# Kernel optimization log

Hardware: AMD Instinct MI355X
Metric: run time of the kernel (lower is better)

## Reference

```python
import jax, jax.numpy as jnp
import numpy as np
from jax import lax

H = 16  # hidden size

def lstm_dir(x_tbd, Wih, Whh, bih, bhh):
    # x_tbd: [T, B, D] -> outputs [T, B, H], final h [B, H]
    T, B, _ = x_tbd.shape
    xg = jnp.einsum('tbd,gd->tbg', x_tbd, Wih) + bih + bhh  # [T, B, 4H]
    def step(carry, xt):
        h, c = carry
        g = xt + h @ Whh.T
        i, f, gg, o = jnp.split(g, 4, axis=-1)  # PyTorch gate order i,f,g,o
        i = jax.nn.sigmoid(i); f = jax.nn.sigmoid(f)
        gg = jnp.tanh(gg); o = jax.nn.sigmoid(o)
        c = f * c + i * gg
        h = o * jnp.tanh(c)
        return (h, c), h
    init = (jnp.zeros((B, H), x_tbd.dtype), jnp.zeros((B, H), x_tbd.dtype))
    (hT, cT), hs = lax.scan(step, init, xg)
    return hs, hT

def bi_layer(x_tbd, pf, pb):
    hs_f, hT_f = lstm_dir(x_tbd, *pf)
    hs_b_rev, hT_b = lstm_dir(x_tbd[::-1], *pb)
    out = jnp.concatenate([hs_f, hs_b_rev[::-1]], axis=-1)  # [T, B, 2H]
    return out, hT_f, hT_b


def setup_inputs() -> dict:
    key = jax.random.key(0)
    ks = iter(jax.random.split(key, 32))
    B, T = 4096, 512
    d = {"x": jax.random.normal(next(ks), (B, T), jnp.float32)}
    def w(shape):
        return jax.random.normal(next(ks), shape, jnp.float32) * 0.2
    # layer 0 (input dim 1), forward / backward directions
    for s in ('f', 'b'):
        d[f'Wih0{s}'] = w((4 * H, 1)); d[f'Whh0{s}'] = w((4 * H, H))
        d[f'bih0{s}'] = jnp.zeros((4 * H,), jnp.float32)
        d[f'bhh0{s}'] = jnp.zeros((4 * H,), jnp.float32)
    # layer 1 (input dim 2H = 32)
    for s in ('f', 'b'):
        d[f'Wih1{s}'] = w((4 * H, 2 * H)); d[f'Whh1{s}'] = w((4 * H, H))
        d[f'bih1{s}'] = jnp.zeros((4 * H,), jnp.float32)
        d[f'bhh1{s}'] = jnp.zeros((4 * H,), jnp.float32)
    # MLP head: Linear(32,25), Linear(25,20)
    d['W1'] = w((25, 2 * H)); d['b1'] = jnp.zeros((25,), jnp.float32)
    d['W2'] = w((20, 25)); d['b2'] = jnp.zeros((20,), jnp.float32)
    return d


def reference(x, Wih0f, Whh0f, bih0f, bhh0f, Wih0b, Whh0b, bih0b, bhh0b,
              Wih1f, Whh1f, bih1f, bhh1f, Wih1b, Whh1b, bih1b, bhh1b,
              W1, b1, W2, b2):
    # x: [B, T] -> unsqueeze(2) -> [B, T, 1]; scan over time, so transpose to [T, B, 1]
    x_tbd = x.T[:, :, None]
    o0, _, _ = bi_layer(x_tbd, (Wih0f, Whh0f, bih0f, bhh0f), (Wih0b, Whh0b, bih0b, bhh0b))
    # dropout=0.1 between layers is inactive in eval mode (reference = eval)
    _, hT_f, hT_b = bi_layer(o0, (Wih1f, Whh1f, bih1f, bhh1f), (Wih1b, Whh1b, bih1b, bhh1b))
    # torch: cat((h[-1], h[-2]), 1) = (last-layer backward, last-layer forward)
    feat = jnp.concatenate([hT_b, hT_f], axis=1)  # [B, 32]
    z = jax.nn.elu(feat)
    z = jax.nn.elu(z @ W1.T + b1)
    z = jax.nn.elu(z @ W2.T + b2)
    return z  # [B, 20]
```

## Files before the change

kernel.cpp:

```cpp
#include <hip/hip_runtime.h>
#include <stdint.h>

#define TT 512
#define BB 4096
#define NT8 512
#define LOG2E 1.4426950408889634f

typedef _Float16 half8_t __attribute__((ext_vector_type(8)));
typedef __fp16 fp16x2_t __attribute__((ext_vector_type(2)));
typedef float f32x4 __attribute__((ext_vector_type(4)));
typedef float f32x2 __attribute__((ext_vector_type(2)));

union FragU { uint4 u4; half8_t h8; };
union PkU { fp16x2_t h2; unsigned int u; };

__device__ __forceinline__ float rcp_(float x){ return __builtin_amdgcn_rcpf(x); }
__device__ __forceinline__ float exp2_(float x){ return __builtin_amdgcn_exp2f(x); }
__device__ __forceinline__ float elu_(float x){ return x > 0.0f ? x : (exp2_(x * LOG2E) - 1.0f); }
__device__ __forceinline__ int mini_(int a, int b){ return a < b ? a : b; }
__device__ __forceinline__ float maskhi_(float x){ return __uint_as_float(__float_as_uint(x) & 0xFFFFE000u); }
__device__ __forceinline__ unsigned int pkrtz_(float a, float b){
    PkU p; p.h2 = __builtin_amdgcn_cvt_pkrtz(a, b); return p.u;
}
__device__ __forceinline__ unsigned int pkrne_(float a, float b){
    PkU p; p.h2[0] = (__fp16)a; p.h2[1] = (__fp16)b; return p.u;
}

__device__ __forceinline__ f32x4 MFMA(half8_t a, half8_t b, f32x4 c) {
    return __builtin_amdgcn_mfma_f32_16x16x32_f16(a, b, c, 0, 0, 0);
}

__device__ __forceinline__ f32x4 ld4_(const float* p){ return *(const f32x4*)p; }

__device__ __forceinline__ half8_t packA8s(const float* s, float sc) {
    half8_t h;
#pragma unroll
    for (int k = 0; k < 8; ++k) h[k] = (_Float16)(s[k] * sc);
    return h;
}
__device__ __forceinline__ half8_t zero8_() {
    half8_t h;
#pragma unroll
    for (int k = 0; k < 8; ++k) h[k] = (_Float16)0.0f;
    return h;
}

__device__ __forceinline__ void cell2p_(f32x2 gi, f32x2 gf, f32x2 gg, f32x2 go,
                                        f32x2& c, f32x2& h) {
    f32x2 ei, ef, eg, eo;
    ei[0] = exp2_(-gi[0]); ei[1] = exp2_(-gi[1]);
    ef[0] = exp2_(-gf[0]); ef[1] = exp2_(-gf[1]);
    eg[0] = exp2_(-gg[0]); eg[1] = exp2_(-gg[1]);
    eo[0] = exp2_(-go[0]); eo[1] = exp2_(-go[1]);
    const f32x2 one = {1.0f, 1.0f};
    f32x2 ai = one + ei, af = one + ef, ag = one + eg, ao = one + eo;
    f32x2 pif = ai * af, pgo = ag * ao;
    f32x2 P = pif * pgo;
    f32x2 R; R[0] = rcp_(P[0]); R[1] = rcp_(P[1]);
    f32x2 I = R * (af * pgo);
    f32x2 F = R * (ai * pgo);
    f32x2 Gt = R * (pif * ao);
    f32x2 O = R * (pif * ag);
    f32x2 G = Gt + Gt - one;
    c = F * c + I * G;
    f32x2 ct = c * (-2.0f * LOG2E);
    f32x2 et; et[0] = exp2_(ct[0]); et[1] = exp2_(ct[1]);
    f32x2 den = one + et;
    f32x2 Rt; Rt[0] = rcp_(den[0]); Rt[1] = rcp_(den[1]);
    f32x2 T = Rt + Rt - one;
    h = O * T;
}


struct PA {
    const float *x;
    const float *WihF, *WhhF, *bihF, *bhhF;
    const float *WihB, *WhhB, *bihB, *bhhB;
    char* ws;
};

__global__ __launch_bounds__(256) void phaseA_k(PA p) {
    __shared__ uint4 ldsAll[4 * 16];
    const int tid = threadIdx.x;
    const int lane = tid & 63;
    const int wv   = tid >> 6;
    char* lds = (char*)ldsAll + wv * 256;
    const int q = lane >> 4, b = lane & 15, c = b & 7;
    const bool hi8 = b >= 8;
    const int chain = blockIdx.x * 4 + wv;
    const int tile = chain >> 1, dir = chain & 1;

    const float* Wih = dir ? p.WihB : p.WihF;
    const float* Whh = dir ? p.WhhB : p.WhhF;
    const float* bih = dir ? p.bihB : p.bihF;
    const float* bhh = dir ? p.bhhB : p.bhhF;

    auto mkA = [&](int m, float sc)->half8_t {
        if (q < 2) return packA8s(Whh + (16*m + b)*16 + 8*q, sc);
        half8_t h = zero8_();
        if (q == 2) {
            float w = Wih[16*m + b] * sc;
            h[0] = (_Float16)w;
            h[1] = (_Float16)w;
        }
        return h;
    };
    half8_t A0 = mkA(0, LOG2E);
    half8_t A1 = mkA(1, LOG2E);
    half8_t A2 = mkA(2, 2.0f*LOG2E);
    half8_t A3 = mkA(3, LOG2E);

    f32x4 bias0 = (ld4_(bih +      4*q) + ld4_(bhh +      4*q)) * LOG2E;
    f32x4 bias1 = (ld4_(bih + 16 + 4*q) + ld4_(bhh + 16 + 4*q)) * LOG2E;
    f32x4 bias2 = (ld4_(bih + 32 + 4*q) + ld4_(bhh + 32 + 4*q)) * (2.0f*LOG2E);
    f32x4 bias3 = (ld4_(bih + 48 + 4*q) + ld4_(bhh + 48 + 4*q)) * LOG2E;

    const int uu  = 4*q + (hi8 ? 2 : 0);
    const int who = c*32 + uu*2;
    const int rdo = c*32 + (q&1)*16;
    const bool qlt2 = q < 2;

    ((unsigned int*)lds)[lane & 63] = 0u;
    __builtin_amdgcn_wave_barrier();

    f32x2 cc = {0.f, 0.f};

    const char* xbase = (const char*)p.x + (size_t)tile*8*TT*4;
    const int   xoff  = c*TT*4;
    char*       wsbase = p.ws + (size_t)tile*TT*512;
    const int   woff  = c*64 + dir*32 + uu*2;

    auto xld = [&](int s_)->float {
        int s = mini_(s_, TT-1);
        int t = dir ? (TT-1-s) : s;
        return *(const float*)(xbase + (size_t)t*4 + xoff);
    };

    auto step = [&](float xv, int t) {
        float mh = maskhi_(xv);
        unsigned int xp = pkrtz_(mh, xv - mh);
        FragU hf; hf.u4 = *(const uint4*)(lds + rdo);
        hf.u4.x = qlt2 ? hf.u4.x : xp;
        f32x4 r0 = MFMA(A0, hf.h8, bias0);
        f32x4 r1 = MFMA(A1, hf.h8, bias1);
        f32x4 r2 = MFMA(A2, hf.h8, bias2);
        f32x4 r3 = MFMA(A3, hf.h8, bias3);
        f32x2 gi, gf, gg, go;
        gi[0] = hi8 ? r0[2] : r0[0]; gi[1] = hi8 ? r0[3] : r0[1];
        gf[0] = hi8 ? r1[2] : r1[0]; gf[1] = hi8 ? r1[3] : r1[1];
        gg[0] = hi8 ? r2[2] : r2[0]; gg[1] = hi8 ? r2[3] : r2[1];
        go[0] = hi8 ? r3[2] : r3[0]; go[1] = hi8 ? r3[3] : r3[1];
        f32x2 hv;
        cell2p_(gi, gf, gg, go, cc, hv);
        unsigned int hh = pkrne_(hv[0], hv[1]);
        *(unsigned int*)(lds + who) = hh;
        *(unsigned int*)(wsbase + (size_t)t*512 + woff) = hh;
        __builtin_amdgcn_wave_barrier();
    };

    float xv0 = xld(0), xv1 = xld(1), xv2 = xld(2), xv3 = xld(3);
    for (int s = 0; s < TT; s += 4) {
        const int t0 = dir ? (TT-1-s) : s;
        const int d  = dir ? -1 : 1;
        step(xv0, t0      ); xv0 = xld(s+4);
        step(xv1, t0 + d  ); xv1 = xld(s+5);
        step(xv2, t0 + 2*d); xv2 = xld(s+6);
        step(xv3, t0 + 3*d); xv3 = xld(s+7);
    }
}

struct PB {
    const float *WihF, *WhhF, *bihF, *bhhF;
    const float *WihB, *WhhB, *bihB, *bhhB;
    const char* ws;
    float* hT;
};

__global__ __launch_bounds__(256) void phaseB_k(PB p) {
    __shared__ uint4 ldsAll[4 * 16];
    const int tid = threadIdx.x;
    const int lane = tid & 63;
    const int wv   = tid >> 6;
    char* lds = (char*)ldsAll + wv * 256;
    const int q = lane >> 4, b = lane & 15, c = b & 7;
    const bool hi8 = b >= 8;
    const int chain = blockIdx.x * 4 + wv;
    const int tile = chain >> 1, dir = chain & 1;

    const float* Wih = dir ? p.WihB : p.WihF;
    const float* Whh = dir ? p.WhhB : p.WhhF;
    const float* bih = dir ? p.bihB : p.bihF;
    const float* bhh = dir ? p.bhhB : p.bhhF;

    const float SC0 = LOG2E, SC1 = LOG2E, SC2 = 2.0f*LOG2E, SC3 = LOG2E;

    half8_t wi0 = packA8s(Wih + (     b)*32 + 8*q, SC0);
    half8_t wi1 = packA8s(Wih + (16 + b)*32 + 8*q, SC1);
    half8_t wi2 = packA8s(Wih + (32 + b)*32 + 8*q, SC2);
    half8_t wi3 = packA8s(Wih + (48 + b)*32 + 8*q, SC3);

    half8_t wh0 = (q < 2) ? packA8s(Whh + (     b)*16 + 8*q, SC0) : zero8_();
    half8_t wh1 = (q < 2) ? packA8s(Whh + (16 + b)*16 + 8*q, SC1) : zero8_();
    half8_t wh2 = (q < 2) ? packA8s(Whh + (32 + b)*16 + 8*q, SC2) : zero8_();
    half8_t wh3 = (q < 2) ? packA8s(Whh + (48 + b)*16 + 8*q, SC3) : zero8_();

    f32x4 bias0 = (ld4_(bih +      4*q) + ld4_(bhh +      4*q)) * SC0;
    f32x4 bias1 = (ld4_(bih + 16 + 4*q) + ld4_(bhh + 16 + 4*q)) * SC1;
    f32x4 bias2 = (ld4_(bih + 32 + 4*q) + ld4_(bhh + 32 + 4*q)) * SC2;
    f32x4 bias3 = (ld4_(bih + 48 + 4*q) + ld4_(bhh + 48 + 4*q)) * SC3;

    const int uu  = 4*q + (hi8 ? 2 : 0);
    const int who = c*32 + uu*2;
    const int rdo = c*32 + (q&1)*16;

    ((unsigned int*)lds)[lane & 63] = 0u;
    __builtin_amdgcn_wave_barrier();

    f32x2 cc = {0.f, 0.f};
    f32x2 hv = {0.f, 0.f};

    const char* wsbase = p.ws + (size_t)tile*TT*512;
    const int   xoff   = c*64 + q*16;

    auto xld = [&](int s_)->uint4 {
        int s = mini_(s_, TT-1);
        int t = dir ? (TT-1-s) : s;
        return *(const uint4*)(wsbase + (size_t)t*512 + xoff);
    };

    auto wiM = [&](uint4 xin, f32x4& o0, f32x4& o1, f32x4& o2, f32x4& o3) {
        FragU xf; xf.u4 = xin;
        o0 = MFMA(wi0, xf.h8, bias0);
        o1 = MFMA(wi1, xf.h8, bias1);
        o2 = MFMA(wi2, xf.h8, bias2);
        o3 = MFMA(wi3, xf.h8, bias3);
    };

    auto stepWh = [&](f32x4 p0, f32x4 p1, f32x4 p2, f32x4 p3) {
        FragU hf; hf.u4 = *(const uint4*)(lds + rdo);
        f32x4 r0 = MFMA(wh0, hf.h8, p0);
        f32x4 r1 = MFMA(wh1, hf.h8, p1);
        f32x4 r2 = MFMA(wh2, hf.h8, p2);
        f32x4 r3 = MFMA(wh3, hf.h8, p3);
        f32x2 gi, gf, gg, go;
        gi[0] = hi8 ? r0[2] : r0[0]; gi[1] = hi8 ? r0[3] : r0[1];
        gf[0] = hi8 ? r1[2] : r1[0]; gf[1] = hi8 ? r1[3] : r1[1];
        gg[0] = hi8 ? r2[2] : r2[0]; gg[1] = hi8 ? r2[3] : r2[1];
        go[0] = hi8 ? r3[2] : r3[0]; go[1] = hi8 ? r3[3] : r3[1];
        cell2p_(gi, gf, gg, go, cc, hv);
        unsigned int hh = pkrne_(hv[0], hv[1]);
        *(unsigned int*)(lds + who) = hh;
        __builtin_amdgcn_wave_barrier();
    };

    uint4 xb0 = xld(0), xb1 = xld(1), xb2 = xld(2), xb3 = xld(3);
    f32x4 pa0, pa1, pa2, pa3, pb0, pb1, pb2, pb3;
    wiM(xb0, pa0, pa1, pa2, pa3);
    for (int s = 0; s < TT; s += 4) {
        wiM(xb1, pb0, pb1, pb2, pb3);
        stepWh(pa0, pa1, pa2, pa3);
        xb0 = xld(s+4);
        wiM(xb2, pa0, pa1, pa2, pa3);
        stepWh(pb0, pb1, pb2, pb3);
        xb1 = xld(s+5);
        wiM(xb3, pb0, pb1, pb2, pb3);
        stepWh(pa0, pa1, pa2, pa3);
        xb2 = xld(s+6);
        wiM(xb0, pa0, pa1, pa2, pa3);
        stepWh(pb0, pb1, pb2, pb3);
        xb3 = xld(s+7);
    }

    const int batch = tile*8 + c;
    float* hp = p.hT + ((size_t)(dir ? BB : 0) + batch)*16 + uu;
    float2 ho; ho.x = hv[0]; ho.y = hv[1];
    *(float2*)hp = ho;
}

struct PC {
    const float* hT;
    const float *W1, *b1, *W2, *b2;
    float* out;
};

__global__ __launch_bounds__(64) void head_k(PC p) {
    const int B = blockIdx.x * 64 + threadIdx.x;
    const float* hf = p.hT + (size_t)B*16;
    const float* hb = p.hT + ((size_t)BB + B)*16;

    float z0[32];
#pragma unroll
    for (int k = 0; k < 16; ++k) z0[k] = elu_(hb[k]);
#pragma unroll
    for (int k = 0; k < 16; ++k) z0[16+k] = elu_(hf[k]);

    float z1[25];
#pragma unroll
    for (int o = 0; o < 25; ++o) {
        float a = p.b1[o];
#pragma unroll
        for (int k = 0; k < 32; ++k) a = fmaf(p.W1[o*32 + k], z0[k], a);
        z1[o] = elu_(a);
    }
#pragma unroll
    for (int o = 0; o < 20; ++o) {
        float a = p.b2[o];
#pragma unroll
        for (int k = 0; k < 25; ++k) a = fmaf(p.W2[o*25 + k], z1[k], a);
        p.out[(size_t)B*20 + o] = elu_(a);
    }
}

extern "C" void kernel_launch(void* const* d_in, const int* in_sizes, int n_in,
                              void* d_out, int out_size, void* d_ws, size_t ws_size,
                              hipStream_t stream) {
    (void)in_sizes; (void)n_in; (void)out_size;

    const size_t frag_bytes = (size_t)NT8 * TT * 512;
    const size_t hT_bytes   = (size_t)2 * BB * 16 * sizeof(float);
    size_t hT_off = (ws_size >= frag_bytes + hT_bytes) ? frag_bytes
                                                       : (ws_size - hT_bytes);
    char* ws = (char*)d_ws;
    float* hT = (float*)(ws + hT_off);

    PA pa;
    pa.x = (const float*)d_in[0];
    pa.WihF = (const float*)d_in[1];  pa.WhhF = (const float*)d_in[2];
    pa.bihF = (const float*)d_in[3];  pa.bhhF = (const float*)d_in[4];
    pa.WihB = (const float*)d_in[5];  pa.WhhB = (const float*)d_in[6];
    pa.bihB = (const float*)d_in[7];  pa.bhhB = (const float*)d_in[8];
    pa.ws = ws;
    hipLaunchKernelGGL(phaseA_k, dim3(256), dim3(256), 0, stream, pa);

    PB pb;
    pb.WihF = (const float*)d_in[9];   pb.WhhF = (const float*)d_in[10];
    pb.bihF = (const float*)d_in[11];  pb.bhhF = (const float*)d_in[12];
    pb.WihB = (const float*)d_in[13];  pb.WhhB = (const float*)d_in[14];
    pb.bihB = (const float*)d_in[15];  pb.bhhB = (const float*)d_in[16];
    pb.ws = ws; pb.hT = hT;
    hipLaunchKernelGGL(phaseB_k, dim3(256), dim3(256), 0, stream, pb);

    PC pc;
    pc.hT = hT;
    pc.W1 = (const float*)d_in[17]; pc.b1 = (const float*)d_in[18];
    pc.W2 = (const float*)d_in[19]; pc.b2 = (const float*)d_in[20];
    pc.out = (float*)d_out;
    hipLaunchKernelGGL(head_k, dim3(BB/64), dim3(64), 0, stream, pc);
}
```

Before: 279.8 us.

## Process four batch columns per wave in phase A to double chain parallelism

Layer-0 recurrence now handles 4 batch columns per wave instead of 8, with each lane computing one hidden unit for one column, and the grid doubles to 512 blocks. This shortens the per-step cell work (one scalar cell per lane instead of two) and doubles the number of concurrent chains to raise occupancy on the latency-bound sequential loop. The x input is now written into LDS each step with an extra wave barrier, and each lane stores fp16 halves individually, which adds LDS and global store traffic per step. Half of each MFMA's B-operand columns are unused.

```diff
diff --git a/kernel.cpp b/kernel.cpp
--- a/kernel.cpp
+++ b/kernel.cpp
@@ -43,6 +43,28 @@
 #pragma unroll
     for (int k = 0; k < 8; ++k) h[k] = (_Float16)0.0f;
     return h;
+}
+
+__device__ __forceinline__ float sel4_(f32x4 a, int j) {
+    float lo = (j & 1) ? a[1] : a[0];
+    float hi = (j & 1) ? a[3] : a[2];
+    return (j & 2) ? hi : lo;
+}
+
+__device__ __forceinline__ float cell1_(float gi, float gf, float gg, float go, float& c) {
+    float ei = exp2_(-gi), ef = exp2_(-gf), eg = exp2_(-gg), eo = exp2_(-go);
+    float ai = 1.0f + ei, af = 1.0f + ef, ag = 1.0f + eg, ao = 1.0f + eo;
+    float p2 = ai * af, p3 = p2 * ag, P = p3 * ao;
+    float R  = rcp_(P);
+    float sgo = ag * ao;
+    float I = R * (af * sgo);
+    float F = R * (ai * sgo);
+    float G = fmaf(2.0f, R * (p2 * ao), -1.0f);
+    float O = R * p3;
+    c = fmaf(F, c, I * G);
+    float et = exp2_(c * (-2.0f * LOG2E));
+    float T  = fmaf(2.0f, rcp_(1.0f + et), -1.0f);
+    return O * T;
 }
 
 __device__ __forceinline__ void cell2p_(f32x2 gi, f32x2 gf, f32x2 gg, f32x2 go,
@@ -80,13 +102,12 @@
 };
 
 __global__ __launch_bounds__(256) void phaseA_k(PA p) {
-    __shared__ uint4 ldsAll[4 * 16];
+    __shared__ uint4 lds4[4 * 20];
     const int tid = threadIdx.x;
     const int lane = tid & 63;
     const int wv   = tid >> 6;
-    char* lds = (char*)ldsAll + wv * 256;
-    const int q = lane >> 4, b = lane & 15, c = b & 7;
-    const bool hi8 = b >= 8;
+    char* lds = (char*)lds4 + wv * 320;
+    const int q = lane >> 4, b = lane & 15, c = b & 3, j = b >> 2;
     const int chain = blockIdx.x * 4 + wv;
     const int tile = chain >> 1, dir = chain & 1;
 
@@ -115,20 +136,22 @@
     f32x4 bias2 = (ld4_(bih + 32 + 4*q) + ld4_(bhh + 32 + 4*q)) * (2.0f*LOG2E);
     f32x4 bias3 = (ld4_(bih + 48 + 4*q) + ld4_(bhh + 48 + 4*q)) * LOG2E;
 
-    const int uu  = 4*q + (hi8 ? 2 : 0);
-    const int who = c*32 + uu*2;
-    const int rdo = c*32 + (q&1)*16;
-    const bool qlt2 = q < 2;
-
-    ((unsigned int*)lds)[lane & 63] = 0u;
+    const int u   = 4*q + j;
+    const int rdo = c*80 + q*16;
+    const int who = c*80 + u*2;
+    const int xwo = c*80 + 32;
+    const bool xw = (q == 2) && (j == 0);
+
+    { unsigned int* z = (unsigned int*)lds;
+      for (int k = lane; k < 80; k += 64) z[k] = 0u; }
     __builtin_amdgcn_wave_barrier();
 
-    f32x2 cc = {0.f, 0.f};
-
-    const char* xbase = (const char*)p.x + (size_t)tile*8*TT*4;
+    float cC = 0.f;
+
+    const char* xbase = (const char*)p.x + (size_t)tile*4*TT*4;
     const int   xoff  = c*TT*4;
-    char*       wsbase = p.ws + (size_t)tile*TT*512;
-    const int   woff  = c*64 + dir*32 + uu*2;
+    char*       wsbase = p.ws + (size_t)(tile >> 1)*TT*512;
+    const int   woff  = ((tile & 1)*4 + c)*64 + dir*32 + u*2;
 
     auto xld = [&](int s_)->float {
         int s = mini_(s_, TT-1);
@@ -139,22 +162,17 @@
     auto step = [&](float xv, int t) {
         float mh = maskhi_(xv);
         unsigned int xp = pkrtz_(mh, xv - mh);
+        if (xw) *(unsigned int*)(lds + xwo) = xp;
+        __builtin_amdgcn_wave_barrier();
         FragU hf; hf.u4 = *(const uint4*)(lds + rdo);
-        hf.u4.x = qlt2 ? hf.u4.x : xp;
         f32x4 r0 = MFMA(A0, hf.h8, bias0);
         f32x4 r1 = MFMA(A1, hf.h8, bias1);
         f32x4 r2 = MFMA(A2, hf.h8, bias2);
         f32x4 r3 = MFMA(A3, hf.h8, bias3);
-        f32x2 gi, gf, gg, go;
-        gi[0] = hi8 ? r0[2] : r0[0]; gi[1] = hi8 ? r0[3] : r0[1];
-        gf[0] = hi8 ? r1[2] : r1[0]; gf[1] = hi8 ? r1[3] : r1[1];
-        gg[0] = hi8 ? r2[2] : r2[0]; gg[1] = hi8 ? r2[3] : r2[1];
-        go[0] = hi8 ? r3[2] : r3[0]; go[1] = hi8 ? r3[3] : r3[1];
-        f32x2 hv;
-        cell2p_(gi, gf, gg, go, cc, hv);
-        unsigned int hh = pkrne_(hv[0], hv[1]);
-        *(unsigned int*)(lds + who) = hh;
-        *(unsigned int*)(wsbase + (size_t)t*512 + woff) = hh;
+        float h = cell1_(sel4_(r0, j), sel4_(r1, j), sel4_(r2, j), sel4_(r3, j), cC);
+        __fp16 h16 = (__fp16)h;
+        *(__fp16*)(lds + who) = h16;
+        *(__fp16*)(wsbase + (size_t)t*512 + woff) = h16;
         __builtin_amdgcn_wave_barrier();
     };
 
@@ -330,7 +348,7 @@
     pa.WihB = (const float*)d_in[5];  pa.WhhB = (const float*)d_in[6];
     pa.bihB = (const float*)d_in[7];  pa.bhhB = (const float*)d_in[8];
     pa.ws = ws;
-    hipLaunchKernelGGL(phaseA_k, dim3(256), dim3(256), 0, stream, pa);
+    hipLaunchKernelGGL(phaseA_k, dim3(512), dim3(256), 0, stream, pa);
 
     PB pb;
     pb.WihF = (const float*)d_in[9];   pb.WhhF = (const float*)d_in[10];
```

Measured after the change: 312.8 us. +11.8%, slower.
